# Kernel tuning notes

Hardware: AMD Instinct MI355X
Metric: run time of the kernel (lower is better)

## Reference

```python
import jax, jax.numpy as jnp
import numpy as np

K = 2  # top-k experts per token


def setup_inputs() -> dict:
    key = jax.random.key(0)
    kx, kw = jax.random.split(key)
    N, D, E = 16384, 4096, 64
    x = jax.random.normal(kx, (N, D), dtype=jnp.float32)
    # nn.Linear(input_dim, num_experts, bias=False) weight: [num_experts, input_dim]
    W = jax.random.normal(kw, (E, D), dtype=jnp.float32) * (1.0 / np.sqrt(D))
    return {"x": x, "W": W}


def reference(x, W):
    # logits = x @ W^T : [N, E]
    logits = jnp.einsum('nd,ed->ne', x, W)
    top_k_logits, top_k_indices = jax.lax.top_k(logits, K)  # [N, K]
    top_k_weights = jax.nn.softmax(top_k_logits, axis=-1)   # softmax over the k selected
    N = logits.shape[0]
    rows = jnp.arange(N)[:, None]  # [N, 1] broadcast against [N, K]
    full_weights = jnp.zeros_like(logits).at[rows, top_k_indices].set(top_k_weights)
    return full_weights, top_k_indices
```

## Files before the change

### kernel.cpp

```cpp
#include <hip/hip_runtime.h>
#include <math.h>

#define N_TOK 16384
#define DDIM  4096
#define NEXP  64
#define TM    32
#define NQ    4
#define KQ    (DDIM / NQ)
#define BKQ   32
#define NSTEP (KQ / BKQ)
#define LSTR  68
#define TAU   1e-3f

typedef __attribute__((ext_vector_type(8))) short bf16x8;
typedef __attribute__((ext_vector_type(4))) float f32x4;

__device__ __forceinline__ void split8(f32x4 v0, f32x4 v1, bf16x8& hi, bf16x8& lo) {
    float f[8];
    *(f32x4*)&f[0] = v0;  *(f32x4*)&f[4] = v1;
    #pragma unroll
    for (int i = 0; i < 8; ++i) {
        unsigned u  = __float_as_uint(f[i]);
        unsigned uh = u & 0xFFFF0000u;
        float    rf = f[i] - __uint_as_float(uh);
        hi[i] = (short)(u >> 16);
        lo[i] = (short)(__float_as_uint(rf) >> 16);
    }
}

__device__ __forceinline__ void gl2lds16(const void* g, void* l) {
    __builtin_amdgcn_global_load_lds(
        (const __attribute__((address_space(1))) unsigned int*)g,
        (__attribute__((address_space(3))) unsigned int*)l,
        16, 0, 0);
}

__global__ __launch_bounds__(256) void pack_w_kernel(
    const float* __restrict__ W, short* __restrict__ Wp)
{
    const int c    = blockIdx.x;
    const int tid  = threadIdx.x;
    const int t    = tid >> 6;
    const int lane = tid & 63;
    const int r16  = lane & 15;
    const int koct = lane >> 4;
    const float* src = W + (size_t)(t * 16 + r16) * DDIM + c * 32 + koct * 8;
    f32x4 b0 = *(const f32x4*)src;
    f32x4 b1 = *(const f32x4*)(src + 4);
    bf16x8 hi, lo;
    split8(b0, b1, hi, lo);
    short* d = Wp + ((size_t)(c * 4 + t) * 2) * 512 + lane * 8;
    *(bf16x8*)d         = hi;
    *(bf16x8*)(d + 512) = lo;
}

__global__ __launch_bounds__(512, 4) void topk_gate_kernel(
    const float* __restrict__ x, const short* __restrict__ Wp,
    const float* __restrict__ W, float* __restrict__ out)
{
    __shared__ __align__(16) char sraw[4 * 16384];
    __shared__ int    top_i[TM * 2];
    __shared__ float  top_w[TM * 2];
    __shared__ int    nflag;
    __shared__ int    flist[TM];
    __shared__ double lgd[NEXP];
    __shared__ int    rbi[2];
    __shared__ float  rbw[2];

    const int tid  = threadIdx.x;
    const int lane = tid & 63;
    const int w    = tid >> 6;
    const int block_tok = blockIdx.x * TM;

    if (w >= 4) {
        const int p  = w - 4;
        const int sw = (((lane & 7) ^ (lane >> 3)) << 4);
        const char* s0 = (const char*)x
            + (size_t)(block_tok + (lane >> 3)) * (DDIM * 4)
            + p * (KQ * 4)
            + sw;
        char* const dq = sraw + (p << 12);

#define STAGE(S) do {                                                        \
        char* _d = dq + (((S) & 3) << 14);                                   \
        const char* _s = s0 + (size_t)(S) * (BKQ * 4);                       \
        gl2lds16(_s,                  _d);                                   \
        gl2lds16(_s + 8  * 16384UL,   _d + 1024);                            \
        gl2lds16(_s + 16 * 16384UL,   _d + 2048);                            \
        gl2lds16(_s + 24 * 16384UL,   _d + 3072);                            \
    } while (0)

        STAGE(0); STAGE(1); STAGE(2);
        asm volatile("s_waitcnt vmcnt(8)" ::: "memory");
        __builtin_amdgcn_s_barrier();
        #pragma unroll 4
        for (int s = 0; s < NSTEP - 3; ++s) {
            STAGE(s + 3);
            asm volatile("s_waitcnt vmcnt(8)" ::: "memory");
            __builtin_amdgcn_s_barrier();
        }
        asm volatile("s_waitcnt vmcnt(4)" ::: "memory");
        __builtin_amdgcn_s_barrier();
        asm volatile("s_waitcnt vmcnt(0)" ::: "memory");
        __builtin_amdgcn_s_barrier();
        __builtin_amdgcn_s_barrier();
#undef STAGE
    } else {
        const int h    = w;
        const int r16  = lane & 15;
        const int koct = lane >> 4;
        const int q4   = (lane & 7) << 4;

        f32x4 acc[2][4];
        #pragma unroll
        for (int tt = 0; tt < 2; ++tt)
            #pragma unroll
            for (int t = 0; t < 4; ++t) acc[tt][t] = (f32x4){0.f, 0.f, 0.f, 0.f};

        __syncthreads();
        #pragma unroll 4
        for (int s = 0; s < NSTEP; ++s) {
            const char* bbase = sraw + ((s & 3) << 14) + (h << 12);
            bf16x8 ah[2], al[2];
            #pragma unroll
            for (int tt = 0; tt < 2; ++tt) {
                const char* xb = bbase + ((tt * 16 + r16) << 7);
                f32x4 a0 = *(const f32x4*)(xb + ((koct * 32)      ^ q4));
                f32x4 a1 = *(const f32x4*)(xb + ((koct * 32 + 16) ^ q4));
                split8(a0, a1, ah[tt], al[tt]);
            }
            const int cg = h * NSTEP + s;
            #pragma unroll
            for (int t = 0; t < 4; ++t) {
                const short* wb = Wp + ((size_t)(cg * 4 + t) * 2) * 512 + lane * 8;
                bf16x8 bh = *(const bf16x8*)wb;
                bf16x8 bl = *(const bf16x8*)(wb + 512);
                #pragma unroll
                for (int tt = 0; tt < 2; ++tt) {
                    acc[tt][t] = __builtin_amdgcn_mfma_f32_16x16x32_bf16(ah[tt], bh, acc[tt][t], 0, 0, 0);
                    acc[tt][t] = __builtin_amdgcn_mfma_f32_16x16x32_bf16(ah[tt], bl, acc[tt][t], 0, 0, 0);
                    acc[tt][t] = __builtin_amdgcn_mfma_f32_16x16x32_bf16(al[tt], bh, acc[tt][t], 0, 0, 0);
                }
            }
            __syncthreads();
        }
        float* Lg = (float*)sraw;
        #pragma unroll
        for (int tt = 0; tt < 2; ++tt)
            #pragma unroll
            for (int t = 0; t < 4; ++t)
                #pragma unroll
                for (int r = 0; r < 4; ++r)
                    Lg[(h * TM + tt * 16 + koct * 4 + r) * LSTR + t * 16 + r16] = acc[tt][t][r];
    }

    if (tid == 0) nflag = 0;
    __syncthreads();

    float* Lg = (float*)sraw;
    {
        const int tok = tid >> 4;
        const int e4  = (tid & 15) * 4;
        float4 s0 = *(float4*)&Lg[(0 * TM + tok) * LSTR + e4];
        #pragma unroll
        for (int qq = 1; qq < 4; ++qq) {
            float4 v = *(float4*)&Lg[(qq * TM + tok) * LSTR + e4];
            s0.x += v.x; s0.y += v.y; s0.z += v.z; s0.w += v.w;
        }
        *(float4*)&Lg[tok * LSTR + e4] = s0;
    }
    __syncthreads();

    if (tid < TM) {
        float m1 = -INFINITY, m2 = -INFINITY, m3 = -INFINITY;
        int i1 = 0, i2 = 0;
        for (int e = 0; e < NEXP; ++e) {
            float v = Lg[tid * LSTR + e];
            if (v > m1)      { m3 = m2; m2 = m1; i2 = i1; m1 = v; i1 = e; }
            else if (v > m2) { m3 = m2; m2 = v; i2 = e; }
            else if (v > m3) { m3 = v; }
        }
        float d  = expf(m2 - m1);
        float rn = 1.0f / (1.0f + d);
        top_i[tid * 2 + 0] = i1;  top_i[tid * 2 + 1] = i2;
        top_w[tid * 2 + 0] = rn;  top_w[tid * 2 + 1] = d * rn;
        float2* oi = (float2*)(out + (size_t)N_TOK * NEXP);
        oi[block_tok + tid] = make_float2((float)i1, (float)i2);
        if ((m1 - m2 < TAU) || (m2 - m3 < TAU)) {
            int pp = atomicAdd(&nflag, 1);
            flist[pp] = tid;
        }
    }
    __syncthreads();

    {
        float4* ow = (float4*)(out + (size_t)block_tok * NEXP);
        const int tok = tid >> 4;
        const int e4  = (tid & 15) * 4;
        int a1 = top_i[tok * 2], a2 = top_i[tok * 2 + 1];
        float v1 = top_w[tok * 2], v2 = top_w[tok * 2 + 1];
        float4 v; float* vp = (float*)&v;
        #pragma unroll
        for (int q = 0; q < 4; ++q) {
            int e = e4 + q;
            vp[q] = (e == a1) ? v1 : ((e == a2) ? v2 : 0.0f);
        }
        ow[tid] = v;
    }
    __syncthreads();

    double* red = (double*)(sraw + 40960);
    const int fn = nflag;
    for (int f = 0; f < fn; ++f) {
        const int tok = block_tok + flist[f];
        {
            const int e = tid & 63, q = tid >> 6;
            const float* wr = W + (size_t)e * DDIM + q * (DDIM / 8);
            const float* xr = x + (size_t)tok * DDIM + q * (DDIM / 8);
            double pp = 0.0;
            for (int k = 0; k < DDIM / 8; k += 4) {
                float4 wv = *(const float4*)(wr + k);
                float4 xv = *(const float4*)(xr + k);
                pp += (double)xv.x * (double)wv.x;
                pp += (double)xv.y * (double)wv.y;
                pp += (double)xv.z * (double)wv.z;
                pp += (double)xv.w * (double)wv.w;
            }
            red[tid] = pp;
        }
        __syncthreads();
        if (tid < 64) {
            double s = 0.0;
            #pragma unroll
            for (int j = 0; j < 8; ++j) s += red[tid + 64 * j];
            lgd[tid] = s;
        }
        __syncthreads();

        if (tid == 0) {
            double m1 = -INFINITY, m2 = -INFINITY;
            int i1 = 0, i2 = 0;
            for (int ee = 0; ee < NEXP; ++ee) {
                double v = lgd[ee];
                if (v > m1)      { m2 = m1; i2 = i1; m1 = v; i1 = ee; }
                else if (v > m2) { m2 = v; i2 = ee; }
            }
            double d  = exp(m2 - m1);
            double rn = 1.0 / (1.0 + d);
            rbi[0] = i1; rbi[1] = i2;
            rbw[0] = (float)rn; rbw[1] = (float)(d * rn);
            float2* oi = (float2*)(out + (size_t)N_TOK * NEXP);
            oi[tok] = make_float2((float)i1, (float)i2);
        }
        __syncthreads();

        if (tid < 16) {
            float4 v = make_float4(0.f, 0.f, 0.f, 0.f);
            float* vp = (float*)&v;
            #pragma unroll
            for (int qq = 0; qq < 4; ++qq) {
                int ee = tid * 4 + qq;
                if (ee == rbi[0]) vp[qq] = rbw[0];
                else if (ee == rbi[1]) vp[qq] = rbw[1];
            }
            ((float4*)(out + (size_t)tok * NEXP))[tid] = v;
        }
        __syncthreads();
    }
}

extern "C" void kernel_launch(void* const* d_in, const int* in_sizes, int n_in,
                              void* d_out, int out_size, void* d_ws, size_t ws_size,
                              hipStream_t stream) {
    const float* x = (const float*)d_in[0];
    const float* W = (const float*)d_in[1];
    float* out = (float*)d_out;
    short* Wp  = (short*)d_ws;
    (void)in_sizes; (void)n_in; (void)ws_size; (void)out_size;

    hipLaunchKernelGGL(pack_w_kernel, dim3(DDIM / 32), dim3(256), 0, stream, W, Wp);
    hipLaunchKernelGGL(topk_gate_kernel, dim3(N_TOK / TM), dim3(512), 0, stream,
                       x, Wp, W, out);
}
```

Baseline: 544.5 us.

## Stage full-row 1KB x windows per step instead of per-warp K-quarter slices

Producer warps now load contiguous 1KB chunks of 8 token rows per stage (256 floats per row, 32KB per stage buffer), replacing the old scheme where each warp streamed its own quarter of K in 128-byte pieces. Consumer warps each handle two 32-column chunks of the shared window, with a new XOR swizzle. The aim is longer contiguous global reads and fewer pipeline steps. In exchange, LDS usage doubles to 128KB and launch bounds drop to 2 blocks per SM, which lowers occupancy.

```diff
diff --git a/kernel.cpp b/kernel.cpp
--- a/kernel.cpp
+++ b/kernel.cpp
@@ -5,10 +5,8 @@
 #define DDIM  4096
 #define NEXP  64
 #define TM    32
-#define NQ    4
-#define KQ    (DDIM / NQ)
-#define BKQ   32
-#define NSTEP (KQ / BKQ)
+#define WINF  256
+#define NSTEP (DDIM / WINF)
 #define LSTR  68
 #define TAU   1e-3f
 
@@ -54,11 +52,11 @@
     *(bf16x8*)(d + 512) = lo;
 }
 
-__global__ __launch_bounds__(512, 4) void topk_gate_kernel(
+__global__ __launch_bounds__(512, 2) void topk_gate_kernel(
     const float* __restrict__ x, const short* __restrict__ Wp,
     const float* __restrict__ W, float* __restrict__ out)
 {
-    __shared__ __align__(16) char sraw[4 * 16384];
+    __shared__ __align__(16) char sraw[4 * 32768];
     __shared__ int    top_i[TM * 2];
     __shared__ float  top_w[TM * 2];
     __shared__ int    nflag;
@@ -73,33 +71,33 @@
     const int block_tok = blockIdx.x * TM;
 
     if (w >= 4) {
-        const int p  = w - 4;
-        const int sw = (((lane & 7) ^ (lane >> 3)) << 4);
-        const char* s0 = (const char*)x
-            + (size_t)(block_tok + (lane >> 3)) * (DDIM * 4)
-            + p * (KQ * 4)
-            + sw;
-        char* const dq = sraw + (p << 12);
+        const int p = w - 4;
+        const char* xs[8];
+        #pragma unroll
+        for (int j = 0; j < 8; ++j)
+            xs[j] = (const char*)x
+                  + (size_t)(block_tok + p * 8 + j) * (DDIM * 4)
+                  + ((lane * 16) ^ (j << 4));
+        const int drow = p * 8 * 1024;
 
 #define STAGE(S) do {                                                        \
-        char* _d = dq + (((S) & 3) << 14);                                   \
-        const char* _s = s0 + (size_t)(S) * (BKQ * 4);                       \
-        gl2lds16(_s,                  _d);                                   \
-        gl2lds16(_s + 8  * 16384UL,   _d + 1024);                            \
-        gl2lds16(_s + 16 * 16384UL,   _d + 2048);                            \
-        gl2lds16(_s + 24 * 16384UL,   _d + 3072);                            \
+        char* _d = sraw + (((S) & 3) << 15) + drow;                          \
+        const size_t _o = (size_t)(S) * 1024;                                \
+        _Pragma("unroll")                                                    \
+        for (int j = 0; j < 8; ++j)                                          \
+            gl2lds16(xs[j] + _o, _d + j * 1024);                             \
     } while (0)
 
         STAGE(0); STAGE(1); STAGE(2);
-        asm volatile("s_waitcnt vmcnt(8)" ::: "memory");
-        __builtin_amdgcn_s_barrier();
-        #pragma unroll 4
+        asm volatile("s_waitcnt vmcnt(16)" ::: "memory");
+        __builtin_amdgcn_s_barrier();
+        #pragma unroll 1
         for (int s = 0; s < NSTEP - 3; ++s) {
             STAGE(s + 3);
-            asm volatile("s_waitcnt vmcnt(8)" ::: "memory");
+            asm volatile("s_waitcnt vmcnt(16)" ::: "memory");
             __builtin_amdgcn_s_barrier();
         }
-        asm volatile("s_waitcnt vmcnt(4)" ::: "memory");
+        asm volatile("s_waitcnt vmcnt(8)" ::: "memory");
         __builtin_amdgcn_s_barrier();
         asm volatile("s_waitcnt vmcnt(0)" ::: "memory");
         __builtin_amdgcn_s_barrier();
@@ -109,7 +107,7 @@
         const int h    = w;
         const int r16  = lane & 15;
         const int koct = lane >> 4;
-        const int q4   = (lane & 7) << 4;
+        const int m    = (r16 & 7) << 4;
 
         f32x4 acc[2][4];
         #pragma unroll
@@ -118,28 +116,33 @@
             for (int t = 0; t < 4; ++t) acc[tt][t] = (f32x4){0.f, 0.f, 0.f, 0.f};
 
         __syncthreads();
-        #pragma unroll 4
+        #pragma unroll 2
         for (int s = 0; s < NSTEP; ++s) {
-            const char* bbase = sraw + ((s & 3) << 14) + (h << 12);
-            bf16x8 ah[2], al[2];
-            #pragma unroll
-            for (int tt = 0; tt < 2; ++tt) {
-                const char* xb = bbase + ((tt * 16 + r16) << 7);
-                f32x4 a0 = *(const f32x4*)(xb + ((koct * 32)      ^ q4));
-                f32x4 a1 = *(const f32x4*)(xb + ((koct * 32 + 16) ^ q4));
-                split8(a0, a1, ah[tt], al[tt]);
-            }
-            const int cg = h * NSTEP + s;
-            #pragma unroll
-            for (int t = 0; t < 4; ++t) {
-                const short* wb = Wp + ((size_t)(cg * 4 + t) * 2) * 512 + lane * 8;
-                bf16x8 bh = *(const bf16x8*)wb;
-                bf16x8 bl = *(const bf16x8*)(wb + 512);
+            const char* buf = sraw + ((s & 3) << 15);
+            #pragma unroll
+            for (int cc = 0; cc < 2; ++cc) {
+                const int c  = h * 2 + cc;
+                const int cg = s * 8 + c;
+                const int o0 = c * 128 + koct * 32;
+                bf16x8 ah[2], al[2];
                 #pragma unroll
                 for (int tt = 0; tt < 2; ++tt) {
-                    acc[tt][t] = __builtin_amdgcn_mfma_f32_16x16x32_bf16(ah[tt], bh, acc[tt][t], 0, 0, 0);
-                    acc[tt][t] = __builtin_amdgcn_mfma_f32_16x16x32_bf16(ah[tt], bl, acc[tt][t], 0, 0, 0);
-                    acc[tt][t] = __builtin_amdgcn_mfma_f32_16x16x32_bf16(al[tt], bh, acc[tt][t], 0, 0, 0);
+                    const char* xb = buf + ((tt * 16 + r16) << 10);
+                    f32x4 a0 = *(const f32x4*)(xb + (o0 ^ m));
+                    f32x4 a1 = *(const f32x4*)(xb + ((o0 + 16) ^ m));
+                    split8(a0, a1, ah[tt], al[tt]);
+                }
+                #pragma unroll
+                for (int t = 0; t < 4; ++t) {
+                    const short* wb = Wp + ((size_t)(cg * 4 + t) * 2) * 512 + lane * 8;
+                    bf16x8 bh = *(const bf16x8*)wb;
+                    bf16x8 bl = *(const bf16x8*)(wb + 512);
+                    #pragma unroll
+                    for (int tt = 0; tt < 2; ++tt) {
+                        acc[tt][t] = __builtin_amdgcn_mfma_f32_16x16x32_bf16(ah[tt], bh, acc[tt][t], 0, 0, 0);
+                        acc[tt][t] = __builtin_amdgcn_mfma_f32_16x16x32_bf16(ah[tt], bl, acc[tt][t], 0, 0, 0);
+                        acc[tt][t] = __builtin_amdgcn_mfma_f32_16x16x32_bf16(al[tt], bh, acc[tt][t], 0, 0, 0);
+                    }
                 }
             }
             __syncthreads();
```

Result: faster. 494.9 us (-9.1%).
